# Optimization experiments

Hardware: AMD Instinct MI355X
Metric: run time of the kernel (lower is better)

## Reference

```python
import jax, jax.numpy as jnp
import numpy as np

Nx, Ny, Nu, Np = 8, 8, 2, 4
DELTA = 0.01
P = dict(alphaA=3.5, alphaB=1.1, pho=5.0, Cp=3.0, Ar=1.0, Ab=1.0,
         kr=1.0, kb=1.0, delH1=10.0, E1byR=3000.0, k1star=2.0e4,
         Td=310.0, Qr=200.0, Qb=200.0, CAf=1.0, Tf=320.0)
YMEAN = jnp.array([0.7, 0.5, 0.5, 310.0, 0.7, 0.5, 0.5, 310.0], jnp.float32)
YSTD  = jnp.array([0.3, 0.2, 0.2, 5.0, 0.3, 0.2, 0.2, 5.0], jnp.float32)
UMEAN = jnp.array([1.0, 0.5], jnp.float32)
USTD  = jnp.array([0.1, 0.05], jnp.float32)


def _fg(x, u):
    """Grey-box CSTR+flash ODE RHS in scaled coordinates. x:(B,8), u:(B,2)."""
    x = x * YSTD + YMEAN
    u = u * USTD + UMEAN
    Hr, CAr, CBr, Tr = x[..., 0:1], x[..., 1:2], x[..., 2:3], x[..., 3:4]
    Hb, CAb, CBb, Tb = x[..., 4:5], x[..., 5:6], x[..., 6:7], x[..., 7:8]
    F, D = u[..., 0:1], u[..., 1:2]
    den = P['alphaA'] * CAb + P['alphaB'] * CBb
    CAd = P['alphaA'] * CAb / den
    CBd = P['alphaB'] * CBb / den
    Fr = P['kr'] * jnp.sqrt(Hr)
    Fb = P['kb'] * jnp.sqrt(Hb)
    k1 = P['k1star'] * jnp.exp(-P['E1byR'] / Tr)
    r1 = k1 * CAr
    dHr  = (F + D - Fr) / P['Ar']
    dCAr = (F * (P['CAf'] - CAr) + D * (CAd - CAr)) / (P['Ar'] * Hr) - r1
    dCBr = (-F * CBr + D * (CBd - CBr)) / (P['Ar'] * Hr) + r1
    dTr  = (F * (P['Tf'] - Tr) + D * (P['Td'] - Tr)) / (P['Ar'] * Hr) \
           - P['Qr'] / (P['pho'] * P['Ar'] * P['Cp'] * Hr) \
           + r1 * P['delH1'] / (P['pho'] * P['Cp'])
    dHb  = (Fr - Fb - D) / P['Ab']
    dCAb = (Fr * (CAr - CAb) + D * (CAb - CAd)) / (P['Ab'] * Hb)
    dCBb = (Fr * (CBr - CBb) + D * (CBb - CBd)) / (P['Ab'] * Hb)
    dTb  = Fr * (Tr - Tb) / (P['Ab'] * Hb) + P['Qb'] / (P['pho'] * P['Ab'] * P['Cp'] * Hb)
    xdot = jnp.concatenate([dHr, dCAr, dCBr, dTr, dHb, dCAb, dCBb, dTb], axis=-1)
    return xdot / YSTD


def _fnn(h, Ws, bs):
    for W, b in zip(Ws[:-1], bs[:-1]):
        h = jnp.tanh(h @ W + b)
    return h @ Ws[-1] + bs[-1]


def _interp(yseq):
    # (B,(Np+1)*Ny) -> midpoint interpolation -> (B, Np*Ny)
    B = yseq.shape[0]
    y = yseq.reshape(B, Np + 1, Ny)
    return (0.5 * (y[:, :-1] + y[:, 1:])).reshape(B, Np * Ny)


def _cell(Ws, bs, xGz, u):
    xG, z = xGz[:, :Nx], xGz[:, Nx:]
    ypseq, upseq = z[:, :Np * Ny], z[:, Np * Ny:]
    k1 = _fg(xG, u) + _fnn(jnp.concatenate([xG, z, u], -1), Ws, bs)
    zi = jnp.concatenate([_interp(jnp.concatenate([ypseq, xG], -1)), upseq], -1)
    x2 = xG + DELTA * (k1 / 2)
    k2 = _fg(x2, u) + _fnn(jnp.concatenate([x2, zi, u], -1), Ws, bs)
    x3 = xG + DELTA * (k2 / 2)
    k3 = _fg(x3, u) + _fnn(jnp.concatenate([x3, zi, u], -1), Ws, bs)
    ypseqShifted = jnp.concatenate([ypseq[:, Ny:], xG], -1)
    zs = jnp.concatenate([ypseqShifted, upseq], -1)
    x4 = xG + DELTA * k3
    k4 = _fg(x4, u) + _fnn(jnp.concatenate([x4, zs, u], -1), Ws, bs)
    y = xG
    xGplus = xG + (DELTA / 6.0) * (k1 + 2 * k2 + 2 * k3 + k4)
    zplus = jnp.concatenate([ypseqShifted, upseq[:, Nu:], u], -1)
    return jnp.concatenate([xGplus, zplus], -1), y


def setup_inputs() -> dict:
    key = jax.random.key(0)
    ks = jax.random.split(key, 8)
    B, T = 8192, 256
    useq = jax.random.uniform(ks[0], (B, T, Nu), dtype=jnp.float32)
    xGz0 = jax.random.uniform(ks[1], (B, Nx + Np * (Ny + Nu)), dtype=jnp.float32)
    W1 = jax.random.normal(ks[2], (50, 64), jnp.float32) * (1.0 / np.sqrt(50.0))
    b1 = jnp.zeros((64,), jnp.float32)
    W2 = jax.random.normal(ks[3], (64, 64), jnp.float32) * (1.0 / 8.0)
    b2 = jnp.zeros((64,), jnp.float32)
    W3 = jax.random.normal(ks[4], (64, 8), jnp.float32) * 1e-3  # near-zero final kernel
    b3 = jnp.zeros((8,), jnp.float32)
    return {"useq": useq, "xGz0": xGz0, "W1": W1, "b1": b1,
            "W2": W2, "b2": b2, "W3": W3, "b3": b3}


def reference(useq, xGz0, W1, b1, W2, b2, W3, b3):
    Ws, bs = (W1, W2, W3), (b1, b2, b3)
    def step(carry, u_t):
        return _cell(Ws, bs, carry, u_t)
    _, ys = jax.lax.scan(step, xGz0, jnp.swapaxes(useq, 0, 1))  # ys: (T,B,Ny)
    return jnp.swapaxes(ys, 0, 1)  # (B,T,Ny)
```

## Files before the change

kernel.cpp:

```cpp
#include <hip/hip_runtime.h>


typedef _Float16 h2_t __attribute__((ext_vector_type(2)));
typedef _Float16 h8_t __attribute__((ext_vector_type(8)));
typedef __fp16  pk2_t __attribute__((ext_vector_type(2)));
typedef float f4_t __attribute__((ext_vector_type(4)));
typedef float f8_t __attribute__((ext_vector_type(8)));
typedef int   i4_t __attribute__((ext_vector_type(4)));

union H2I { h2_t h; pk2_t p; int i; float _f; };

#define DEVI __device__ __forceinline__

DEVI float rcp_f(float x) { return __builtin_amdgcn_rcpf(x); }
#if __has_builtin(__builtin_amdgcn_exp2f)
DEVI float exp2_f(float x) { return __builtin_amdgcn_exp2f(x); }
#else
DEVI float exp2_f(float x) { return __expf(x * 0.69314718056f); }
#endif
DEVI int pkrtz_i(float a, float b) { H2I u; u.p = __builtin_amdgcn_cvt_pkrtz(a, b); return u.i; }
DEVI int h2i(h2_t h) { H2I u; u.h = h; return u.i; }
DEVI h2_t i2h(int i) { H2I u; u.i = i; return u.h; }

#if __has_builtin(__builtin_elementwise_fma)
DEVI f8_t fma8(f8_t a, f8_t b, f8_t c) { return __builtin_elementwise_fma(a, b, c); }
#else
DEVI f8_t fma8(f8_t a, f8_t b, f8_t c) {
    f8_t r;
#pragma unroll
    for (int i = 0; i < 8; ++i) r[i] = fmaf(a[i], b[i], c[i]);
    return r;
}
#endif
DEVI f8_t splat8(float v) { f8_t r = { v, v, v, v, v, v, v, v }; return r; }

DEVI f4_t mfma16(h8_t a, h8_t b, f4_t c) {
    return __builtin_amdgcn_mfma_f32_16x16x32_f16(a, b, c, 0, 0, 0);
}

DEVI int chan_of(int ct, int rho) {
    int qr = rho >> 2, rr = rho & 3;
    return (ct < 2) ? (8 * qr + 4 * ct + rr)
                    : (32 + 8 * qr + 4 * (ct - 2) + rr);
}

DEVI f8_t fg_eval(f8_t x, float F, float D) {
    const f8_t ystd  = { 0.3f, 0.2f, 0.2f, 5.0f, 0.3f, 0.2f, 0.2f, 5.0f };
    const f8_t ymean = { 0.7f, 0.5f, 0.5f, 310.0f, 0.7f, 0.5f, 0.5f, 310.0f };
    f8_t xs = fma8(x, ystd, ymean);

    float Hr  = xs[0], CAr = xs[1], CBr = xs[2], Tr = xs[3];
    float Hb  = xs[4], CAb = xs[5], CBb = xs[6], Tb = xs[7];

    float aA = 3.5f * CAb, aB = 1.1f * CBb;
    float rden = rcp_f(aA + aB);
    float CAd = aA * rden, CBd = aB * rden;
    float Fr = __builtin_amdgcn_sqrtf(Hr);
    float Fb = __builtin_amdgcn_sqrtf(Hb);
    float rTr = rcp_f(Tr);
    float k1v = 20000.0f * __expf(-3000.0f * rTr);
    float r1 = k1v * CAr;
    float rHr = rcp_f(Hr), rHb = rcp_f(Hb);

    f8_t d;
    d[0] = F + D - Fr;
    d[1] = (F * (1.0f - CAr) + D * (CAd - CAr)) * rHr - r1;
    d[2] = (D * (CBd - CBr) - F * CBr) * rHr + r1;
    d[3] = (F * (320.0f - Tr) + D * (310.0f - Tr)) * rHr
         - (40.0f / 3.0f) * rHr + (2.0f / 3.0f) * r1;
    d[4] = Fr - Fb - D;
    d[5] = (Fr * (CAr - CAb) + D * (CAb - CAd)) * rHb;
    d[6] = (Fr * (CBr - CBb) + D * (CBb - CBd)) * rHb;
    d[7] = Fr * (Tr - Tb) * rHb + (40.0f / 3.0f) * rHb;

    const f8_t sc = { 10.0f / 3.0f, 5.0f, 5.0f, 0.2f,
                      10.0f / 3.0f, 5.0f, 5.0f, 0.2f };
    return d * sc;
}

struct Weights {
    h8_t a1[4][2], a2[4][2], a3[2];
    f4_t b1f[4], b2f[4], b3f;
};

DEVI int sigpair(float a, float b) {
    float s0 = rcp_f(1.0f + exp2_f(a));
    float s1 = rcp_f(1.0f + exp2_f(b));
    return pkrtz_i(s0, s1);
}

DEVI h8_t sig4(f4_t a0, f4_t a1) {
    i4_t g;
    g[0] = sigpair(a0[0], a0[1]);
    g[1] = sigpair(a0[2], a0[3]);
    g[2] = sigpair(a1[0], a1[1]);
    g[3] = sigpair(a1[2], a1[3]);
    return __builtin_bit_cast(h8_t, g);
}

DEVI i4_t avg4(i4_t A, i4_t B) {
    const h2_t half2c = { (_Float16)0.5f, (_Float16)0.5f };
    i4_t r;
#pragma unroll
    for (int i = 0; i < 4; ++i)
        r[i] = h2i((i2h(A[i]) + i2h(B[i])) * half2c);
    return r;
}

DEVI i4_t sel_f0y(i4_t V0, i4_t V1, i4_t V2, int q) {
    i4_t r;
#pragma unroll
    for (int i = 0; i < 4; ++i) {
        int t = (q == 2) ? V1[i] : V2[i];
        r[i] = (q == 1) ? V0[i] : t;
    }
    return r;
}
DEVI i4_t sel_f1(i4_t V3, i4_t f1c, int q) {
    i4_t r;
#pragma unroll
    for (int i = 0; i < 4; ++i)
        r[i] = (q == 0) ? V3[i] : f1c[i];
    return r;
}

DEVI f8_t eval_stage(f8_t x, i4_t px, i4_t f0y, i4_t f1w,
                     float F, float D, const Weights& W, int q) {
    f8_t kfg = fg_eval(x, F, D);

    i4_t f0w;
#pragma unroll
    for (int i = 0; i < 4; ++i)
        f0w[i] = (q == 0) ? px[i] : f0y[i];
    h8_t f0 = __builtin_bit_cast(h8_t, f0w);
    h8_t f1 = __builtin_bit_cast(h8_t, f1w);

    f4_t a0 = mfma16(W.a1[0][0], f0, W.b1f[0]);
    f4_t a1 = mfma16(W.a1[1][0], f0, W.b1f[1]);
    f4_t a2 = mfma16(W.a1[2][0], f0, W.b1f[2]);
    f4_t a3 = mfma16(W.a1[3][0], f0, W.b1f[3]);
    a0 = mfma16(W.a1[0][1], f1, a0);
    a1 = mfma16(W.a1[1][1], f1, a1);
    a2 = mfma16(W.a1[2][1], f1, a2);
    a3 = mfma16(W.a1[3][1], f1, a3);

    h8_t g0 = sig4(a0, a1);
    f4_t c0 = mfma16(W.a2[0][0], g0, W.b2f[0]);
    f4_t c1 = mfma16(W.a2[1][0], g0, W.b2f[1]);
    f4_t c2 = mfma16(W.a2[2][0], g0, W.b2f[2]);
    f4_t c3 = mfma16(W.a2[3][0], g0, W.b2f[3]);
    h8_t g1 = sig4(a2, a3);
    c0 = mfma16(W.a2[0][1], g1, c0);
    c1 = mfma16(W.a2[1][1], g1, c1);
    c2 = mfma16(W.a2[2][1], g1, c2);
    c3 = mfma16(W.a2[3][1], g1, c3);

    h8_t h0 = sig4(c0, c1);
    f4_t acc3 = mfma16(W.a3[0], h0, W.b3f);
    h8_t h1 = sig4(c2, c3);
    acc3 = mfma16(W.a3[1], h1, acc3);

    f8_t nn;
#pragma unroll
    for (int r = 0; r < 4; ++r) {
        int e = __float_as_int(acc3[r]);
        int o = e;
        asm("v_permlane16_swap_b32 %0, %1" : "+v"(e), "+v"(o));
        nn[r]     = __int_as_float(e);
        nn[4 + r] = __int_as_float(o);
    }

    return kfg + nn;
}

DEVI i4_t pack_pairs(f8_t x) {
    i4_t r;
#pragma unroll
    for (int i = 0; i < 4; ++i) r[i] = pkrtz_i(x[2 * i], x[2 * i + 1]);
    return r;
}

__global__ __launch_bounds__(64, 1)
void cstr_mfma1_kernel(const float* __restrict__ useq, const float* __restrict__ xGz0,
                       const float* __restrict__ W1, const float* __restrict__ b1,
                       const float* __restrict__ W2, const float* __restrict__ b2,
                       const float* __restrict__ W3, const float* __restrict__ b3,
                       float* __restrict__ out)
{
    const int lane = threadIdx.x & 63;
    const int m16 = lane & 15, q = lane >> 4;
    const int b0 = blockIdx.x * 16;

    const float S1 = 2.0f * 1.4426950408889634f;

    Weights W;
#pragma unroll
    for (int ct = 0; ct < 4; ++ct) {
        const int n = chan_of(ct, m16);
#pragma unroll
        for (int kh = 0; kh < 2; ++kh) {
            i4_t w1f, w2f;
#pragma unroll
            for (int jj = 0; jj < 4; ++jj) {
                int k0 = 32 * kh + 8 * q + 2 * jj;
                int k1 = k0 + 1;
                float v1a = (k0 < 50) ? S1 * W1[k0 * 64 + n] : 0.0f;
                float v1b = (k1 < 50) ? S1 * W1[k1 * 64 + n] : 0.0f;
                float v2a = -2.0f * S1 * W2[k0 * 64 + n];
                float v2b = -2.0f * S1 * W2[k1 * 64 + n];
                w1f[jj] = pkrtz_i(v1a, v1b);
                w2f[jj] = pkrtz_i(v2a, v2b);
            }
            W.a1[ct][kh] = __builtin_bit_cast(h8_t, w1f);
            W.a2[ct][kh] = __builtin_bit_cast(h8_t, w2f);
        }
        f4_t bb1, bb2;
#pragma unroll
        for (int r = 0; r < 4; ++r) {
            int ch = chan_of(ct, 4 * q + r);
            bb1[r] = S1 * b1[ch];
            float cs = 0.0f;
            for (int j = 0; j < 64; ++j) cs += W2[j * 64 + ch];
            bb2[r] = S1 * (b2[ch] + cs);
        }
        W.b1f[ct] = bb1;
        W.b2f[ct] = bb2;
    }
#pragma unroll
    for (int kh = 0; kh < 2; ++kh) {
        i4_t w3f;
#pragma unroll
        for (int jj = 0; jj < 4; ++jj) {
            int k0 = 32 * kh + 8 * q + 2 * jj;
            float va = -2.0f * W3[k0 * 8 + (m16 & 7)];
            float vb = -2.0f * W3[(k0 + 1) * 8 + (m16 & 7)];
            w3f[jj] = pkrtz_i(va, vb);
        }
        W.a3[kh] = __builtin_bit_cast(h8_t, w3f);
    }
    {
        f4_t bb3;
#pragma unroll
        for (int r = 0; r < 4; ++r) {
            int c = (4 * q + r) & 7;
            float cs = 0.0f;
            for (int j = 0; j < 64; ++j) cs += W3[j * 8 + c];
            bb3[r] = b3[c] + cs;
        }
        W.b3f = bb3;
    }

    const float* xz = xGz0 + (size_t)(b0 + m16) * 48;
    f8_t xg;
#pragma unroll
    for (int c = 0; c < 8; ++c) xg[c] = xz[c];
    i4_t P0, P1, P2, P3, U;
#pragma unroll
    for (int i = 0; i < 4; ++i) {
        P0[i] = pkrtz_i(xz[ 8 + 2 * i], xz[ 9 + 2 * i]);
        P1[i] = pkrtz_i(xz[16 + 2 * i], xz[17 + 2 * i]);
        P2[i] = pkrtz_i(xz[24 + 2 * i], xz[25 + 2 * i]);
        P3[i] = pkrtz_i(xz[32 + 2 * i], xz[33 + 2 * i]);
        U[i]  = pkrtz_i(xz[40 + 2 * i], xz[41 + 2 * i]);
    }

    const float2* ur = (const float2*)(useq + (size_t)(b0 + m16) * 512);
    float2* ow = (float2*)(out + (size_t)(b0 + m16) * 2048) + q;

    float2 uu = ur[0];

    const f8_t c005  = splat8(0.005f);
    const f8_t c01   = splat8(0.01f);
    const f8_t c2    = splat8(2.0f);
    const f8_t cD6   = splat8(0.0016666667f);

#pragma unroll 1
    for (int t = 0; t < 256; ++t) {
        const float2 uun = ur[(t + 1) & 255];

        {
            float s0 = (q == 0) ? xg[0] : (q == 1) ? xg[2] : (q == 2) ? xg[4] : xg[6];
            float s1 = (q == 0) ? xg[1] : (q == 1) ? xg[3] : (q == 2) ? xg[5] : xg[7];
            float2 st = { s0, s1 };
            ow[t * 4] = st;
        }

        const float u0 = uu.x, u1 = uu.y;
        const float F = fmaf(u0, 0.1f, 1.0f);
        const float D = fmaf(u1, 0.05f, 0.5f);
        const int upair_i = pkrtz_i(u0, u1);

        i4_t XC = pack_pairs(xg);

        i4_t B0 = avg4(P0, P1), B1 = avg4(P1, P2),
             B2 = avg4(P2, P3), B3 = avg4(P3, XC);

        i4_t f1c;
#pragma unroll
        for (int i = 0; i < 4; ++i) {
            int t0 = (i == 0) ? ((q == 2) ? upair_i : 0) : 0;
            f1c[i] = (q == 1) ? U[i] : t0;
        }

        i4_t f0yA = sel_f0y(P0, P1, P2, q), f1A = sel_f1(P3, f1c, q);
        i4_t f0yB = sel_f0y(B0, B1, B2, q), f1B = sel_f1(B3, f1c, q);
        i4_t f0yC = sel_f0y(P1, P2, P3, q), f1C = sel_f1(XC, f1c, q);

        f8_t kc, ks, xv;
        kc = eval_stage(xg, XC, f0yA, f1A, F, D, W, q);
        ks = kc;
        xv = fma8(c005, kc, xg);
        kc = eval_stage(xv, pack_pairs(xv), f0yB, f1B, F, D, W, q);
        ks = fma8(c2, kc, ks);
        xv = fma8(c005, kc, xg);
        kc = eval_stage(xv, pack_pairs(xv), f0yB, f1B, F, D, W, q);
        ks = fma8(c2, kc, ks);
        xv = fma8(c01, kc, xg);
        kc = eval_stage(xv, pack_pairs(xv), f0yC, f1C, F, D, W, q);

        ks = ks + kc;
        xg = fma8(cD6, ks, xg);

        P0 = P1; P1 = P2; P2 = P3; P3 = XC;
        {
            i4_t Un;
            Un[0] = U[1]; Un[1] = U[2]; Un[2] = U[3]; Un[3] = upair_i;
            U = Un;
        }

        uu = uun;
    }
}

extern "C" void kernel_launch(void* const* d_in, const int* in_sizes, int n_in,
                              void* d_out, int out_size, void* d_ws, size_t ws_size,
                              hipStream_t stream) {
    const float* useq = (const float*)d_in[0];
    const float* xGz0 = (const float*)d_in[1];
    const float* W1   = (const float*)d_in[2];
    const float* b1   = (const float*)d_in[3];
    const float* W2   = (const float*)d_in[4];
    const float* b2   = (const float*)d_in[5];
    const float* W3   = (const float*)d_in[6];
    const float* b3   = (const float*)d_in[7];
    float* out = (float*)d_out;

    cstr_mfma1_kernel<<<dim3(512), dim3(64), 0, stream>>>(
        useq, xGz0, W1, b1, W2, b2, W3, b3, out);
}
```

Measured before the change: 806.4 us.

## Precompute state-independent layer-1 contributions and split MFMA accumulation chains

The layer-1 input is split into the state-dependent part (xG, lanes q==0) and the state-independent part (z history, u). The independent part's MFMA products for RK stages 2-4 are computed once per timestep, off the critical path. Each later stage then needs only 4 layer-1 MFMAs instead of 8. Layer-2 and layer-3 accumulation chains are also split into two independent MFMA chains plus a vector add, which shortens the dependent chain latency at the cost of extra adds and registers.

```diff
diff --git a/kernel.cpp b/kernel.cpp
--- a/kernel.cpp
+++ b/kernel.cpp
@@ -124,8 +124,44 @@
     return r;
 }
 
-DEVI f8_t eval_stage(f8_t x, i4_t px, i4_t f0y, i4_t f1w,
-                     float F, float D, const Weights& W, int q) {
+DEVI f8_t stage_tail(f4_t a0, f4_t a1, f4_t a2, f4_t a3,
+                     f8_t kfg, const Weights& W) {
+    const f4_t z4 = { 0.0f, 0.0f, 0.0f, 0.0f };
+
+    h8_t g0 = sig4(a0, a1);
+    h8_t g1 = sig4(a2, a3);
+
+    f4_t c0 = mfma16(W.a2[0][0], g0, W.b2f[0]);
+    f4_t c1 = mfma16(W.a2[1][0], g0, W.b2f[1]);
+    f4_t c2 = mfma16(W.a2[2][0], g0, W.b2f[2]);
+    f4_t c3 = mfma16(W.a2[3][0], g0, W.b2f[3]);
+    f4_t d0 = mfma16(W.a2[0][1], g1, z4);
+    f4_t d1 = mfma16(W.a2[1][1], g1, z4);
+    f4_t d2 = mfma16(W.a2[2][1], g1, z4);
+    f4_t d3 = mfma16(W.a2[3][1], g1, z4);
+    c0 = c0 + d0; c1 = c1 + d1; c2 = c2 + d2; c3 = c3 + d3;
+
+    h8_t h0 = sig4(c0, c1);
+    h8_t h1 = sig4(c2, c3);
+    f4_t e0 = mfma16(W.a3[0], h0, W.b3f);
+    f4_t e1 = mfma16(W.a3[1], h1, z4);
+    f4_t acc3 = e0 + e1;
+
+    f8_t nn;
+#pragma unroll
+    for (int r = 0; r < 4; ++r) {
+        int e = __float_as_int(acc3[r]);
+        int o = e;
+        asm("v_permlane16_swap_b32 %0, %1" : "+v"(e), "+v"(o));
+        nn[r]     = __int_as_float(e);
+        nn[4 + r] = __int_as_float(o);
+    }
+
+    return kfg + nn;
+}
+
+DEVI f8_t eval_stage1(f8_t x, i4_t px, i4_t f0y, i4_t f1w,
+                      float F, float D, const Weights& W, int q) {
     f8_t kfg = fg_eval(x, F, D);
 
     i4_t f0w;
@@ -144,33 +180,26 @@
     a2 = mfma16(W.a1[2][1], f1, a2);
     a3 = mfma16(W.a1[3][1], f1, a3);
 
-    h8_t g0 = sig4(a0, a1);
-    f4_t c0 = mfma16(W.a2[0][0], g0, W.b2f[0]);
-    f4_t c1 = mfma16(W.a2[1][0], g0, W.b2f[1]);
-    f4_t c2 = mfma16(W.a2[2][0], g0, W.b2f[2]);
-    f4_t c3 = mfma16(W.a2[3][0], g0, W.b2f[3]);
-    h8_t g1 = sig4(a2, a3);
-    c0 = mfma16(W.a2[0][1], g1, c0);
-    c1 = mfma16(W.a2[1][1], g1, c1);
-    c2 = mfma16(W.a2[2][1], g1, c2);
-    c3 = mfma16(W.a2[3][1], g1, c3);
-
-    h8_t h0 = sig4(c0, c1);
-    f4_t acc3 = mfma16(W.a3[0], h0, W.b3f);
-    h8_t h1 = sig4(c2, c3);
-    acc3 = mfma16(W.a3[1], h1, acc3);
-
-    f8_t nn;
-#pragma unroll
-    for (int r = 0; r < 4; ++r) {
-        int e = __float_as_int(acc3[r]);
-        int o = e;
-        asm("v_permlane16_swap_b32 %0, %1" : "+v"(e), "+v"(o));
-        nn[r]     = __int_as_float(e);
-        nn[4 + r] = __int_as_float(o);
-    }
-
-    return kfg + nn;
+    return stage_tail(a0, a1, a2, a3, kfg, W);
+}
+
+DEVI f8_t eval_stage_x(f8_t x, i4_t px,
+                       f4_t y0, f4_t y1, f4_t y2, f4_t y3,
+                       float F, float D, const Weights& W, int q) {
+    f8_t kfg = fg_eval(x, F, D);
+
+    i4_t pxf;
+#pragma unroll
+    for (int i = 0; i < 4; ++i)
+        pxf[i] = (q == 0) ? px[i] : 0;
+    h8_t f0x = __builtin_bit_cast(h8_t, pxf);
+
+    f4_t a0 = mfma16(W.a1[0][0], f0x, y0);
+    f4_t a1 = mfma16(W.a1[1][0], f0x, y1);
+    f4_t a2 = mfma16(W.a1[2][0], f0x, y2);
+    f4_t a3 = mfma16(W.a1[3][0], f0x, y3);
+
+    return stage_tail(a0, a1, a2, a3, kfg, W);
 }
 
 DEVI i4_t pack_pairs(f8_t x) {
@@ -306,17 +335,44 @@
         i4_t f0yB = sel_f0y(B0, B1, B2, q), f1B = sel_f1(B3, f1c, q);
         i4_t f0yC = sel_f0y(P1, P2, P3, q), f1C = sel_f1(XC, f1c, q);
 
+        i4_t f0zB, f0zC;
+#pragma unroll
+        for (int i = 0; i < 4; ++i) {
+            f0zB[i] = (q == 0) ? 0 : f0yB[i];
+            f0zC[i] = (q == 0) ? 0 : f0yC[i];
+        }
+        h8_t fzB = __builtin_bit_cast(h8_t, f0zB);
+        h8_t f1Bh = __builtin_bit_cast(h8_t, f1B);
+        h8_t fzC = __builtin_bit_cast(h8_t, f0zC);
+        h8_t f1Ch = __builtin_bit_cast(h8_t, f1C);
+        f4_t yB0 = mfma16(W.a1[0][0], fzB, W.b1f[0]);
+        f4_t yB1 = mfma16(W.a1[1][0], fzB, W.b1f[1]);
+        f4_t yB2 = mfma16(W.a1[2][0], fzB, W.b1f[2]);
+        f4_t yB3 = mfma16(W.a1[3][0], fzB, W.b1f[3]);
+        yB0 = mfma16(W.a1[0][1], f1Bh, yB0);
+        yB1 = mfma16(W.a1[1][1], f1Bh, yB1);
+        yB2 = mfma16(W.a1[2][1], f1Bh, yB2);
+        yB3 = mfma16(W.a1[3][1], f1Bh, yB3);
+        f4_t yC0 = mfma16(W.a1[0][0], fzC, W.b1f[0]);
+        f4_t yC1 = mfma16(W.a1[1][0], fzC, W.b1f[1]);
+        f4_t yC2 = mfma16(W.a1[2][0], fzC, W.b1f[2]);
+        f4_t yC3 = mfma16(W.a1[3][0], fzC, W.b1f[3]);
+        yC0 = mfma16(W.a1[0][1], f1Ch, yC0);
+        yC1 = mfma16(W.a1[1][1], f1Ch, yC1);
+        yC2 = mfma16(W.a1[2][1], f1Ch, yC2);
+        yC3 = mfma16(W.a1[3][1], f1Ch, yC3);
+
         f8_t kc, ks, xv;
-        kc = eval_stage(xg, XC, f0yA, f1A, F, D, W, q);
+        kc = eval_stage1(xg, XC, f0yA, f1A, F, D, W, q);
         ks = kc;
         xv = fma8(c005, kc, xg);
-        kc = eval_stage(xv, pack_pairs(xv), f0yB, f1B, F, D, W, q);
+        kc = eval_stage_x(xv, pack_pairs(xv), yB0, yB1, yB2, yB3, F, D, W, q);
         ks = fma8(c2, kc, ks);
         xv = fma8(c005, kc, xg);
-        kc = eval_stage(xv, pack_pairs(xv), f0yB, f1B, F, D, W, q);
+        kc = eval_stage_x(xv, pack_pairs(xv), yB0, yB1, yB2, yB3, F, D, W, q);
         ks = fma8(c2, kc, ks);
         xv = fma8(c01, kc, xg);
-        kc = eval_stage(xv, pack_pairs(xv), f0yC, f1C, F, D, W, q);
+        kc = eval_stage_x(xv, pack_pairs(xv), yC0, yC1, yC2, yC3, F, D, W, q);
 
         ks = ks + kc;
         xg = fma8(cD6, ks, xg);
```

Result: slower. 888.3 us (+10.2%).
